# Performance work log

Measured on AMD Instinct MI355X. Metric: run time of the kernel, lower is better.

The kernel has to match this reference:

```python
import jax, jax.numpy as jnp
import numpy as np

LIMB_CONNECTION = jnp.array([0, 0, 1, 1, 1, 3, 4, 5, 6, 2, 2, 9, 10, 11, 12], dtype=jnp.int32)


def setup_inputs() -> dict:
    key = jax.random.key(0)
    B, K, D = 1000000, 15, 3
    inputs = jax.random.normal(key, (B, K, D), dtype=jnp.float32)
    return {"inputs": inputs}


def reference(inputs):
    # inputs: [B, 15, 3]. Gather connected keypoint per joint, L2 distance.
    connected = inputs[:, LIMB_CONNECTION, :]          # [B, 15, 3]
    diff = inputs - connected                          # [B, 15, 3]
    limbs = jnp.sqrt(jnp.sum(diff * diff, axis=-1, keepdims=True))  # [B, 15, 1]
    return limbs
```

## Files before the change

### kernel.cpp

```cpp
#include <hip/hip_runtime.h>

#define PERSONS 256
#define ROW 45
#define KJ 15

__global__ __launch_bounds__(256) void limb_kernel(const float* __restrict__ in,
                                                   float* __restrict__ out, int B) {
    __shared__ float lds[PERSONS * ROW];
    const int tid = threadIdx.x;
    const long long bstart = (long long)blockIdx.x * PERSONS;
    const int npersons = (int)min((long long)PERSONS, (long long)B - bstart);
    const long long fbase = bstart * ROW;

    const int F  = npersons * ROW;
    const int Fv = F >> 2;
    const float4* __restrict__ src4 = (const float4*)(in + fbase);
    float4* lds4 = (float4*)lds;
    for (int idx = tid; idx < Fv; idx += 256) lds4[idx] = src4[idx];
    for (int idx = (Fv << 2) + tid; idx < F; idx += 256) lds[idx] = in[fbase + idx];
    __syncthreads();

    float r[KJ];
    const int conn[KJ] = {0, 0, 1, 1, 1, 3, 4, 5, 6, 2, 2, 9, 10, 11, 12};
    if (tid < npersons) {
        const float* s = &lds[tid * ROW];
        #pragma unroll
        for (int k = 0; k < KJ; ++k) {
            const int c = conn[k];
            const float dx = s[k * 3 + 0] - s[c * 3 + 0];
            const float dy = s[k * 3 + 1] - s[c * 3 + 1];
            const float dz = s[k * 3 + 2] - s[c * 3 + 2];
            r[k] = sqrtf(dx * dx + dy * dy + dz * dz);
        }
    }
    __syncthreads();

    if (tid < npersons) {
        #pragma unroll
        for (int k = 0; k < KJ; ++k) lds[tid * KJ + k] = r[k];
    }
    __syncthreads();

    const int G  = npersons * KJ;
    const int Gv = G >> 2;
    float4* __restrict__ dst4 = (float4*)(out + bstart * KJ);
    const float4* lds4c = (const float4*)lds;
    for (int idx = tid; idx < Gv; idx += 256) dst4[idx] = lds4c[idx];
    for (int idx = (Gv << 2) + tid; idx < G; idx += 256) out[bstart * KJ + idx] = lds[idx];
}

extern "C" void kernel_launch(void* const* d_in, const int* in_sizes, int n_in,
                              void* d_out, int out_size, void* d_ws, size_t ws_size,
                              hipStream_t stream) {
    const float* in = (const float*)d_in[0];
    float* out = (float*)d_out;
    const int B = in_sizes[0] / ROW;
    const int grid = (B + PERSONS - 1) / PERSONS;
    limb_kernel<<<grid, 256, 0, stream>>>(in, out, B);
}
```

Baseline: 48.73 us.

## Write limb outputs directly from registers and halve block size

Removes the LDS staging of outputs and the two barriers around it, so each thread writes its 15 results directly to global memory. Block size and persons per block drop to 128, which reduces LDS per block and allows more resident blocks. Coordinates are loaded into registers first. Per-thread strided global stores may coalesce worse than the previous float4 block-contiguous writes.

```diff
diff --git a/kernel.cpp b/kernel.cpp
--- a/kernel.cpp
+++ b/kernel.cpp
@@ -1,10 +1,11 @@
 #include <hip/hip_runtime.h>
 
-#define PERSONS 256
-#define ROW 45
-#define KJ 15
+#define TPB     128
+#define PERSONS 128
+#define ROW     45
+#define KJ      15
 
-__global__ __launch_bounds__(256) void limb_kernel(const float* __restrict__ in,
+__global__ __launch_bounds__(TPB) void limb_kernel(const float* __restrict__ in,
                                                    float* __restrict__ out, int B) {
     __shared__ float lds[PERSONS * ROW];
     const int tid = threadIdx.x;
@@ -16,37 +17,30 @@
     const int Fv = F >> 2;
     const float4* __restrict__ src4 = (const float4*)(in + fbase);
     float4* lds4 = (float4*)lds;
-    for (int idx = tid; idx < Fv; idx += 256) lds4[idx] = src4[idx];
-    for (int idx = (Fv << 2) + tid; idx < F; idx += 256) lds[idx] = in[fbase + idx];
+    for (int idx = tid; idx < Fv; idx += TPB) lds4[idx] = src4[idx];
+    for (int idx = (Fv << 2) + tid; idx < F; idx += TPB) lds[idx] = in[fbase + idx];
     __syncthreads();
 
-    float r[KJ];
-    const int conn[KJ] = {0, 0, 1, 1, 1, 3, 4, 5, 6, 2, 2, 9, 10, 11, 12};
     if (tid < npersons) {
         const float* s = &lds[tid * ROW];
+        float x[KJ], y[KJ], z[KJ];
+        #pragma unroll
+        for (int k = 0; k < KJ; ++k) {
+            x[k] = s[k * 3 + 0];
+            y[k] = s[k * 3 + 1];
+            z[k] = s[k * 3 + 2];
+        }
+        const int conn[KJ] = {0, 0, 1, 1, 1, 3, 4, 5, 6, 2, 2, 9, 10, 11, 12};
+        float* o = out + (bstart + tid) * KJ;
         #pragma unroll
         for (int k = 0; k < KJ; ++k) {
             const int c = conn[k];
-            const float dx = s[k * 3 + 0] - s[c * 3 + 0];
-            const float dy = s[k * 3 + 1] - s[c * 3 + 1];
-            const float dz = s[k * 3 + 2] - s[c * 3 + 2];
-            r[k] = sqrtf(dx * dx + dy * dy + dz * dz);
+            const float dx = x[k] - x[c];
+            const float dy = y[k] - y[c];
+            const float dz = z[k] - z[c];
+            o[k] = sqrtf(dx * dx + dy * dy + dz * dz);
         }
     }
-    __syncthreads();
-
-    if (tid < npersons) {
-        #pragma unroll
-        for (int k = 0; k < KJ; ++k) lds[tid * KJ + k] = r[k];
-    }
-    __syncthreads();
-
-    const int G  = npersons * KJ;
-    const int Gv = G >> 2;
-    float4* __restrict__ dst4 = (float4*)(out + bstart * KJ);
-    const float4* lds4c = (const float4*)lds;
-    for (int idx = tid; idx < Gv; idx += 256) dst4[idx] = lds4c[idx];
-    for (int idx = (Gv << 2) + tid; idx < G; idx += 256) out[bstart * KJ + idx] = lds[idx];
 }
 
 extern "C" void kernel_launch(void* const* d_in, const int* in_sizes, int n_in,
@@ -56,5 +50,5 @@
     float* out = (float*)d_out;
     const int B = in_sizes[0] / ROW;
     const int grid = (B + PERSONS - 1) / PERSONS;
-    limb_kernel<<<grid, 256, 0, stream>>>(in, out, B);
+    limb_kernel<<<grid, TPB, 0, stream>>>(in, out, B);
 }
```

After: 53.66 us. 1.1x slower.
